# Optimization experiments

Measured on AMD Instinct MI355X. Metric: run time of the kernel, lower is better.

The kernel has to match this reference:

```python
import jax, jax.numpy as jnp
import numpy as np

D_MODEL = 1024
N_HEADS = 16


def setup_inputs() -> dict:
    key = jax.random.key(0)
    ks = jax.random.split(key, 11)
    B, L, D = 2, 2048, D_MODEL
    s = 1.0 / np.sqrt(D)
    return {
        "q": jax.random.normal(ks[0], (B, L, D), jnp.float32),
        "k": jax.random.normal(ks[1], (B, L, D), jnp.float32),
        "v": jax.random.normal(ks[2], (B, L, D), jnp.float32),
        "w_q": jax.random.normal(ks[3], (D, D), jnp.float32) * s,
        "b_q": jnp.zeros((D,), jnp.float32),
        "w_k": jax.random.normal(ks[4], (D, D), jnp.float32) * s,
        "b_k": jnp.zeros((D,), jnp.float32),
        "w_v": jax.random.normal(ks[5], (D, D), jnp.float32) * s,
        "b_v": jnp.zeros((D,), jnp.float32),
        "w_o": jax.random.normal(ks[6], (D, D), jnp.float32) * s,
        "b_o": jnp.zeros((D,), jnp.float32),
    }


def reference(q, k, v, w_q, b_q, w_k, b_k, w_v, b_v, w_o, b_o):
    B, L, D = q.shape
    H = N_HEADS
    d_h = D // H
    # QKV projections (nn.Linear: x @ W^T + b)
    qh = (q @ w_q.T + b_q).reshape(B, L, H, d_h).transpose(0, 2, 1, 3)  # [B,H,L,d_h]
    kh = (k @ w_k.T + b_k).reshape(B, L, H, d_h).transpose(0, 2, 1, 3)
    vh = (v @ w_v.T + b_v).reshape(B, L, H, d_h).transpose(0, 2, 1, 3)
    # scaled dot-product attention
    scores = jnp.einsum('bhqd,bhkd->bhqk', qh, kh) / jnp.sqrt(jnp.float32(d_h))
    attn = jax.nn.softmax(scores, axis=-1)                               # [B,H,L,L]
    ctx = jnp.einsum('bhqk,bhkd->bhqd', attn, vh)                        # [B,H,L,d_h]
    ctx = ctx.transpose(0, 2, 1, 3).reshape(B, L, D)
    out = ctx @ w_o.T + b_o
    return out, attn
```

## Files before the change

### kernel.cpp

```cpp
#include <hip/hip_runtime.h>
#include <hip/hip_bf16.h>
#include <stdint.h>

#define DEV static __device__ __forceinline__

typedef float f32x4 __attribute__((ext_vector_type(4)));
typedef __bf16 bf16x8 __attribute__((ext_vector_type(8)));
typedef unsigned short u16x8 __attribute__((ext_vector_type(8)));
typedef unsigned short u16x4 __attribute__((ext_vector_type(4)));
typedef uint32_t u32x2 __attribute__((ext_vector_type(2)));
typedef unsigned short u16;

#define B_ 2
#define L_ 2048
#define D_MODEL_ 1024
#define H_ 16
#define DH_ 64

#define SHIFT2 11.5415603f

DEV u16 f2bf(float f) {
  union { float f; uint32_t u; } v; v.f = f;
  uint32_t r = v.u + 0x7FFFu + ((v.u >> 16) & 1u);
  return (u16)(r >> 16);
}

DEV float exp2v(float x) {
#if __has_builtin(__builtin_amdgcn_exp2f)
  return __builtin_amdgcn_exp2f(x);
#else
  float r;
  asm("v_exp_f32 %0, %1" : "=v"(r) : "v"(x));
  return r;
#endif
}

DEV uint32_t pkbf(float a, float b) {
  __hip_bfloat162 h = __float22bfloat162_rn(float2{a, b});
  union { __hip_bfloat162 h; uint32_t u; } cv; cv.h = h;
  return cv.u;
}

DEV f32x4 mfma16(bf16x8 a, bf16x8 b, f32x4 c) {
  return __builtin_amdgcn_mfma_f32_16x16x32_bf16(a, b, c, 0, 0, 0);
}

DEV void gl_lds16(const void* g, void* l) {
  __builtin_amdgcn_global_load_lds(
      (const __attribute__((address_space(1))) unsigned int*)g,
      (__attribute__((address_space(3))) unsigned int*)l, 16, 0, 0);
}

struct CastArgs {
  const float* src[7];
  u16* dst[7];
  int n8[7];
};

__global__ __launch_bounds__(256) void cast_kernel(CastArgs a) {
  const int z = blockIdx.z;
  const float* s = a.src[z];
  u16* d = a.dst[z];
  const int n8 = a.n8[z];
  const int stride = gridDim.x * blockDim.x;
  for (int i = blockIdx.x * blockDim.x + threadIdx.x; i < n8; i += stride) {
    const float4* sp = (const float4*)s + (size_t)i * 2;
    float4 x0 = sp[0], x1 = sp[1];
    u16x8 o;
    o[0] = f2bf(x0.x); o[1] = f2bf(x0.y); o[2] = f2bf(x0.z); o[3] = f2bf(x0.w);
    o[4] = f2bf(x1.x); o[5] = f2bf(x1.y); o[6] = f2bf(x1.z); o[7] = f2bf(x1.w);
    *((u16x8*)d + i) = o;
  }
}

#define GM 4096
#define GN 1024
#define GK 1024

struct GemmArgs {
  const u16* X[3];
  const u16* W[3];
  const float* bias[3];
  void* out[3];
  float alpha[3];
  int mode[3];
};

__global__ __launch_bounds__(256) void gemm_bt(GemmArgs g) {
  const int z = blockIdx.z;
  const u16* X = g.X[z];
  const u16* W = g.W[z];
  const float* bias = g.bias[z];
  const float alpha = g.alpha[z];
  const int mode = g.mode[z];
  const int m0 = blockIdx.y * 128, n0 = blockIdx.x * 128;

  __shared__ __align__(16) char smem[32 * 1024];
  char* As = smem;
  char* Bs = smem + 16 * 1024;

  const int tid = threadIdx.x;
  const int lane = tid & 63, w = tid >> 6;
  const int l15 = lane & 15, l4 = lane >> 4;
  const int wm = (w >> 1) * 64, wn = (w & 1) * 64;

  f32x4 acc[4][4];
#pragma unroll
  for (int i = 0; i < 4; ++i)
#pragma unroll
    for (int j = 0; j < 4; ++j) acc[i][j] = f32x4{0.f, 0.f, 0.f, 0.f};

  for (int ks = 0; ks < GK; ks += 64) {
    __syncthreads();
    for (int c = w; c < 16; c += 4) {
      int r = c * 8 + (lane >> 3);
      int j = lane & 7;
      int sj = j ^ (r & 7);
      gl_lds16((const char*)(X + (size_t)(m0 + r) * GK + ks) + sj * 16, As + c * 1024);
      gl_lds16((const char*)(W + (size_t)(n0 + r) * GK + ks) + sj * 16, Bs + c * 1024);
    }
    __syncthreads();
#pragma unroll
    for (int ksub = 0; ksub < 2; ++ksub) {
      bf16x8 af[4], bfr[4];
#pragma unroll
      for (int mf = 0; mf < 4; ++mf) {
        int r = wm + mf * 16 + l15;
        int j16 = ksub * 4 + l4;
        af[mf] = *(const bf16x8*)(As + r * 128 + ((j16 ^ (r & 7)) * 16));
      }
#pragma unroll
      for (int nf = 0; nf < 4; ++nf) {
        int r = wn + nf * 16 + l15;
        int j16 = ksub * 4 + l4;
        bfr[nf] = *(const bf16x8*)(Bs + r * 128 + ((j16 ^ (r & 7)) * 16));
      }
#pragma unroll
      for (int mf = 0; mf < 4; ++mf)
#pragma unroll
        for (int nf = 0; nf < 4; ++nf) acc[mf][nf] = mfma16(af[mf], bfr[nf], acc[mf][nf]);
    }
  }

  if (mode == 2) {
    u16* base = (u16*)g.out[z];
#pragma unroll
    for (int nf = 0; nf < 4; ++nf) {
      int n = n0 + wn + nf * 16 + l15;
      float bv = bias[n];
#pragma unroll
      for (int mf = 0; mf < 4; ++mf) {
        int m = m0 + wm + mf * 16 + l4 * 4;
        u16x4 pk;
#pragma unroll
        for (int r = 0; r < 4; ++r) pk[r] = f2bf((acc[mf][nf][r] + bv) * alpha);
        size_t off = (((size_t)(m >> 11) * H_ + (n >> 6)) * DH_ + (n & 63)) * (size_t)L_ + (m & 2047);
        *(u16x4*)(base + off) = pk;
      }
    }
  } else {
#pragma unroll
    for (int nf = 0; nf < 4; ++nf) {
      int n = n0 + wn + nf * 16 + l15;
      float bv = bias[n];
#pragma unroll
      for (int mf = 0; mf < 4; ++mf) {
#pragma unroll
        for (int r = 0; r < 4; ++r) {
          int m = m0 + wm + mf * 16 + l4 * 4 + r;
          float val = (acc[mf][nf][r] + bv) * alpha;
          if (mode == 1)
            ((float*)g.out[z])[(size_t)m * GN + n] = val;
          else
            ((u16*)g.out[z])[(size_t)m * GN + n] = f2bf(val);
        }
      }
    }
  }
}

__global__ __launch_bounds__(256) void attn_kernel(const u16* Qp, const u16* Kp,
                                                   const u16* VT, float* attn,
                                                   u16* ctx) {
  const int q0 = blockIdx.x * 64;
  const int h = blockIdx.y, b = blockIdx.z;
  const int tid = threadIdx.x, lane = tid & 63, w = tid >> 6;
  const int l15 = lane & 15, l4 = lane >> 4;
  const int lr = lane >> 3, lj = lane & 7;

  __shared__ __align__(16) char smem[48 * 1024];
  char* Qs = smem;
  char* Ps = smem + 8192;

  const u16* Qbase = Qp + ((size_t)(b * L_ + q0) * D_MODEL_ + h * DH_);
  const u16* Kbase = Kp + ((size_t)(b * L_) * D_MODEL_ + h * DH_);
  const u16* VTb = VT + ((size_t)((b * H_ + h) * DH_) * L_);
  float* attnb = attn + ((size_t)(b * H_ + h)) * L_ * L_;

  auto stK = [&](int t) {
    const int c0 = t * 64, bsel = (t & 1) << 13;
    for (int c = w; c < 8; c += 4) {
      int r = c * 8 + lr, sj = lj ^ (r & 7);
      gl_lds16((const char*)(Kbase + (size_t)(c0 + r) * D_MODEL_) + sj * 16,
               smem + 16384 + bsel + c * 1024);
    }
  };
  auto stV = [&](int t) {
    const int c0 = t * 64, bsel = (t & 1) << 13;
    for (int c = w; c < 8; c += 4) {
      int r = c * 8 + lr, sj = lj ^ (r & 7);
      gl_lds16((const char*)(VTb + (size_t)r * L_ + c0) + sj * 16,
               smem + 32768 + bsel + c * 1024);
    }
  };

  for (int c = w; c < 8; c += 4) {
    int r = c * 8 + lr, sj = lj ^ (r & 7);
    gl_lds16((const char*)(Qbase + (size_t)r * D_MODEL_) + sj * 16, Qs + c * 1024);
  }
  stK(0);
  __syncthreads();

  bf16x8 qa[2];
#pragma unroll
  for (int ksub = 0; ksub < 2; ++ksub) {
    int r = w * 16 + l15;
    int j16 = ksub * 4 + l4;
    qa[ksub] = *(const bf16x8*)(Qs + r * 128 + ((j16 ^ (r & 7)) * 16));
  }

  float ssum = 0.f;
  for (int t = 0; t < 32; ++t) {
    if (t < 31) stK(t + 1);
    const char* Ks = smem + 16384 + ((t & 1) << 13);
    f32x4 s[4];
#pragma unroll
    for (int nf = 0; nf < 4; ++nf) s[nf] = f32x4{0.f, 0.f, 0.f, 0.f};
    __builtin_amdgcn_s_setprio(1);
#pragma unroll
    for (int ksub = 0; ksub < 2; ++ksub) {
      int j16 = ksub * 4 + l4;
      bf16x8 kb[4];
#pragma unroll
      for (int nf = 0; nf < 4; ++nf) {
        int r = nf * 16 + l15;
        kb[nf] = *(const bf16x8*)(Ks + r * 128 + ((j16 ^ (r & 7)) * 16));
      }
#pragma unroll
      for (int nf = 0; nf < 4; ++nf) s[nf] = mfma16(kb[nf], qa[ksub], s[nf]);
    }
    __builtin_amdgcn_s_setprio(0);
#pragma unroll
    for (int nf = 0; nf < 4; ++nf)
#pragma unroll
      for (int r = 0; r < 4; ++r) ssum += exp2v(s[nf][r] - SHIFT2);
    __syncthreads();
  }

  stK(0);
  stV(0);

  ssum += __shfl_xor(ssum, 16);
  ssum += __shfl_xor(ssum, 32);
  const float c2 = SHIFT2 + __log2f(ssum);

  f32x4 cacc[4];
#pragma unroll
  for (int i = 0; i < 4; ++i) cacc[i] = f32x4{0.f, 0.f, 0.f, 0.f};
  __syncthreads();

  const int rowq = w * 16 + l15;
  char* PsRow = Ps + rowq * 128;
  float* arow = attnb + (size_t)(q0 + rowq) * L_ + 4 * l4;

  for (int t = 0; t < 32; ++t) {
    if (t < 31) { stK(t + 1); stV(t + 1); }
    const char* Ks = smem + 16384 + ((t & 1) << 13);
    const char* Vs = smem + 32768 + ((t & 1) << 13);
    const int c0 = t * 64;
    f32x4 s[4];
#pragma unroll
    for (int nf = 0; nf < 4; ++nf) s[nf] = f32x4{0.f, 0.f, 0.f, 0.f};
    __builtin_amdgcn_s_setprio(1);
#pragma unroll
    for (int ksub = 0; ksub < 2; ++ksub) {
      int j16 = ksub * 4 + l4;
      bf16x8 kb[4];
#pragma unroll
      for (int nf = 0; nf < 4; ++nf) {
        int r = nf * 16 + l15;
        kb[nf] = *(const bf16x8*)(Ks + r * 128 + ((j16 ^ (r & 7)) * 16));
      }
#pragma unroll
      for (int nf = 0; nf < 4; ++nf) s[nf] = mfma16(kb[nf], qa[ksub], s[nf]);
    }
    __builtin_amdgcn_s_setprio(0);
#pragma unroll
    for (int nf = 0; nf < 4; ++nf) {
      float p0 = exp2v(s[nf][0] - c2);
      float p1 = exp2v(s[nf][1] - c2);
      float p2 = exp2v(s[nf][2] - c2);
      float p3 = exp2v(s[nf][3] - c2);
      f32x4 p4 = {p0, p1, p2, p3};
      __builtin_nontemporal_store(p4, (f32x4*)(arow + c0 + 16 * nf));
      int off = nf * 32 + l4 * 8;
      int chunk = (off >> 4) ^ (rowq & 7);
      u32x2 pk;
      pk[0] = pkbf(p0, p1);
      pk[1] = pkbf(p2, p3);
      *(u32x2*)(PsRow + chunk * 16 + (off & 15)) = pk;
    }
    __builtin_amdgcn_s_setprio(1);
#pragma unroll
    for (int ksub = 0; ksub < 2; ++ksub) {
      int j16 = ksub * 4 + l4;
      bf16x8 pa = *(const bf16x8*)(PsRow + ((j16 ^ (rowq & 7)) * 16));
#pragma unroll
      for (int df = 0; df < 4; ++df) {
        int r = df * 16 + l15;
        bf16x8 vb = *(const bf16x8*)(Vs + r * 128 + ((j16 ^ (r & 7)) * 16));
        cacc[df] = mfma16(pa, vb, cacc[df]);
      }
    }
    __builtin_amdgcn_s_setprio(0);
    __syncthreads();
  }

#pragma unroll
  for (int df = 0; df < 4; ++df) {
#pragma unroll
    for (int r = 0; r < 4; ++r) {
      int row = q0 + w * 16 + l4 * 4 + r;
      int col = h * DH_ + df * 16 + l15;
      ctx[(size_t)(b * L_ + row) * D_MODEL_ + col] = f2bf(cacc[df][r]);
    }
  }
}

extern "C" void kernel_launch(void* const* d_in, const int* in_sizes, int n_in,
                              void* d_out, int out_size, void* d_ws, size_t ws_size,
                              hipStream_t stream) {
  const float* q = (const float*)d_in[0];
  const float* k = (const float*)d_in[1];
  const float* v = (const float*)d_in[2];
  const float* w_q = (const float*)d_in[3];
  const float* b_q = (const float*)d_in[4];
  const float* w_k = (const float*)d_in[5];
  const float* b_k = (const float*)d_in[6];
  const float* w_v = (const float*)d_in[7];
  const float* b_v = (const float*)d_in[8];
  const float* w_o = (const float*)d_in[9];
  const float* b_o = (const float*)d_in[10];

  float* out = (float*)d_out;
  float* attn = (float*)d_out + (size_t)B_ * L_ * D_MODEL_;

  const size_t MB = 1u << 20;
  char* ws = (char*)d_ws;
  u16* qb = (u16*)(ws + 0 * MB);
  u16* kb = (u16*)(ws + 8 * MB);
  u16* vb = (u16*)(ws + 16 * MB);
  u16* wqb = (u16*)(ws + 24 * MB);
  u16* wkb = (u16*)(ws + 26 * MB);
  u16* wvb = (u16*)(ws + 28 * MB);
  u16* wob = (u16*)(ws + 30 * MB);
  u16* Qp = (u16*)(ws + 32 * MB);
  u16* Kp = (u16*)(ws + 40 * MB);
  u16* VT = (u16*)(ws + 48 * MB);
  u16* ctx = kb;

  CastArgs ca;
  ca.src[0] = q;   ca.dst[0] = qb;  ca.n8[0] = (B_ * L_ * D_MODEL_) / 8;
  ca.src[1] = k;   ca.dst[1] = kb;  ca.n8[1] = (B_ * L_ * D_MODEL_) / 8;
  ca.src[2] = v;   ca.dst[2] = vb;  ca.n8[2] = (B_ * L_ * D_MODEL_) / 8;
  ca.src[3] = w_q; ca.dst[3] = wqb; ca.n8[3] = (D_MODEL_ * D_MODEL_) / 8;
  ca.src[4] = w_k; ca.dst[4] = wkb; ca.n8[4] = (D_MODEL_ * D_MODEL_) / 8;
  ca.src[5] = w_v; ca.dst[5] = wvb; ca.n8[5] = (D_MODEL_ * D_MODEL_) / 8;
  ca.src[6] = w_o; ca.dst[6] = wob; ca.n8[6] = (D_MODEL_ * D_MODEL_) / 8;
  cast_kernel<<<dim3(1024, 1, 7), 256, 0, stream>>>(ca);

  GemmArgs ga;
  ga.X[0] = qb;  ga.W[0] = wqb; ga.bias[0] = b_q; ga.out[0] = Qp; ga.alpha[0] = 0.125f * 1.44269504f; ga.mode[0] = 0;
  ga.X[1] = kb;  ga.W[1] = wkb; ga.bias[1] = b_k; ga.out[1] = Kp; ga.alpha[1] = 1.f;    ga.mode[1] = 0;
  ga.X[2] = vb;  ga.W[2] = wvb; ga.bias[2] = b_v; ga.out[2] = VT; ga.alpha[2] = 1.f;    ga.mode[2] = 2;
  gemm_bt<<<dim3(8, 32, 3), 256, 0, stream>>>(ga);

  attn_kernel<<<dim3(32, 16, 2), 256, 0, stream>>>(Qp, Kp, VT, attn, ctx);

  GemmArgs go;
  go.X[0] = ctx; go.W[0] = wob; go.bias[0] = b_o; go.out[0] = out; go.alpha[0] = 1.f; go.mode[0] = 1;
  go.X[1] = ctx; go.W[1] = wob; go.bias[1] = b_o; go.out[1] = out; go.alpha[1] = 1.f; go.mode[1] = 1;
  go.X[2] = ctx; go.W[2] = wob; go.bias[2] = b_o; go.out[2] = out; go.alpha[2] = 1.f; go.mode[2] = 1;
  gemm_bt<<<dim3(8, 32, 1), 256, 0, stream>>>(go);
}
```

Measured before the change: 286.5 us.

## Load K/V tiles directly from global into registers and remap blocks by XCD

The attention kernel stops staging Q, K and V tiles through shared memory with async global-to-LDS copies and double buffering. Each wave now loads its MFMA operands straight from global memory (L2) into registers, which removes all block-level barriers and cuts LDS use to 8 KB, used only for the per-wave P tile. The grid is flattened and remapped so that consecutive blocks on the same XCD share a head and batch, aiming for better L2 reuse of K/V. The costs are redundant global loads across the four waves and uncoalesced 16-byte row reads, with less latency hiding, though occupancy may rise.

After: 444.4 us. 1.55x slower.

```diff
diff --git a/kernel.cpp b/kernel.cpp
--- a/kernel.cpp
+++ b/kernel.cpp
@@ -182,83 +182,53 @@
 __global__ __launch_bounds__(256) void attn_kernel(const u16* Qp, const u16* Kp,
                                                    const u16* VT, float* attn,
                                                    u16* ctx) {
-  const int q0 = blockIdx.x * 64;
-  const int h = blockIdx.y, b = blockIdx.z;
+  const int hid = blockIdx.x;
+  const int lid = (hid & 7) * 128 + (hid >> 3);
+  const int q0 = (lid & 31) * 64;
+  const int h = (lid >> 5) & 15;
+  const int b = lid >> 9;
+
   const int tid = threadIdx.x, lane = tid & 63, w = tid >> 6;
   const int l15 = lane & 15, l4 = lane >> 4;
-  const int lr = lane >> 3, lj = lane & 7;
-
-  __shared__ __align__(16) char smem[48 * 1024];
-  char* Qs = smem;
-  char* Ps = smem + 8192;
-
-  const u16* Qbase = Qp + ((size_t)(b * L_ + q0) * D_MODEL_ + h * DH_);
-  const u16* Kbase = Kp + ((size_t)(b * L_) * D_MODEL_ + h * DH_);
-  const u16* VTb = VT + ((size_t)((b * H_ + h) * DH_) * L_);
+
+  __shared__ __align__(16) char smem[8192];
+  char* PsRow = smem + w * 2048 + l15 * 128;
+  const int swz = l15 & 7;
+
+  const u16* Qbase = Qp + ((size_t)(b * L_ + q0 + w * 16) * D_MODEL_ + h * DH_);
+  const u16* Kb = Kp + ((size_t)(b * L_) * D_MODEL_ + h * DH_);
+  const u16* Vb = VT + ((size_t)((b * H_ + h) * DH_) * L_);
   float* attnb = attn + ((size_t)(b * H_ + h)) * L_ * L_;
 
-  auto stK = [&](int t) {
-    const int c0 = t * 64, bsel = (t & 1) << 13;
-    for (int c = w; c < 8; c += 4) {
-      int r = c * 8 + lr, sj = lj ^ (r & 7);
-      gl_lds16((const char*)(Kbase + (size_t)(c0 + r) * D_MODEL_) + sj * 16,
-               smem + 16384 + bsel + c * 1024);
-    }
-  };
-  auto stV = [&](int t) {
-    const int c0 = t * 64, bsel = (t & 1) << 13;
-    for (int c = w; c < 8; c += 4) {
-      int r = c * 8 + lr, sj = lj ^ (r & 7);
-      gl_lds16((const char*)(VTb + (size_t)r * L_ + c0) + sj * 16,
-               smem + 32768 + bsel + c * 1024);
-    }
-  };
-
-  for (int c = w; c < 8; c += 4) {
-    int r = c * 8 + lr, sj = lj ^ (r & 7);
-    gl_lds16((const char*)(Qbase + (size_t)r * D_MODEL_) + sj * 16, Qs + c * 1024);
-  }
-  stK(0);
-  __syncthreads();
-
   bf16x8 qa[2];
 #pragma unroll
-  for (int ksub = 0; ksub < 2; ++ksub) {
-    int r = w * 16 + l15;
-    int j16 = ksub * 4 + l4;
-    qa[ksub] = *(const bf16x8*)(Qs + r * 128 + ((j16 ^ (r & 7)) * 16));
-  }
+  for (int ksub = 0; ksub < 2; ++ksub)
+    qa[ksub] = *(const bf16x8*)(Qbase + (size_t)l15 * D_MODEL_ + (ksub * 4 + l4) * 8);
 
   float ssum = 0.f;
   for (int t = 0; t < 32; ++t) {
-    if (t < 31) stK(t + 1);
-    const char* Ks = smem + 16384 + ((t & 1) << 13);
+    const u16* Kt = Kb + (size_t)t * 64 * D_MODEL_;
+    bf16x8 kb[2][4];
+#pragma unroll
+    for (int ksub = 0; ksub < 2; ++ksub)
+#pragma unroll
+      for (int nf = 0; nf < 4; ++nf)
+        kb[ksub][nf] = *(const bf16x8*)(Kt + (size_t)(nf * 16 + l15) * D_MODEL_ +
+                                        (ksub * 4 + l4) * 8);
     f32x4 s[4];
 #pragma unroll
     for (int nf = 0; nf < 4; ++nf) s[nf] = f32x4{0.f, 0.f, 0.f, 0.f};
     __builtin_amdgcn_s_setprio(1);
 #pragma unroll
-    for (int ksub = 0; ksub < 2; ++ksub) {
-      int j16 = ksub * 4 + l4;
-      bf16x8 kb[4];
-#pragma unroll
-      for (int nf = 0; nf < 4; ++nf) {
-        int r = nf * 16 + l15;
-        kb[nf] = *(const bf16x8*)(Ks + r * 128 + ((j16 ^ (r & 7)) * 16));
-      }
-#pragma unroll
-      for (int nf = 0; nf < 4; ++nf) s[nf] = mfma16(kb[nf], qa[ksub], s[nf]);
-    }
+    for (int ksub = 0; ksub < 2; ++ksub)
+#pragma unroll
+      for (int nf = 0; nf < 4; ++nf) s[nf] = mfma16(kb[ksub][nf], qa[ksub], s[nf]);
     __builtin_amdgcn_s_setprio(0);
 #pragma unroll
     for (int nf = 0; nf < 4; ++nf)
 #pragma unroll
       for (int r = 0; r < 4; ++r) ssum += exp2v(s[nf][r] - SHIFT2);
-    __syncthreads();
-  }
-
-  stK(0);
-  stV(0);
+  }
 
   ssum += __shfl_xor(ssum, 16);
   ssum += __shfl_xor(ssum, 32);
@@ -267,33 +237,30 @@
   f32x4 cacc[4];
 #pragma unroll
   for (int i = 0; i < 4; ++i) cacc[i] = f32x4{0.f, 0.f, 0.f, 0.f};
-  __syncthreads();
-
-  const int rowq = w * 16 + l15;
-  char* PsRow = Ps + rowq * 128;
-  float* arow = attnb + (size_t)(q0 + rowq) * L_ + 4 * l4;
+
+  float* arow = attnb + (size_t)(q0 + w * 16 + l15) * L_ + 4 * l4;
 
   for (int t = 0; t < 32; ++t) {
-    if (t < 31) { stK(t + 1); stV(t + 1); }
-    const char* Ks = smem + 16384 + ((t & 1) << 13);
-    const char* Vs = smem + 32768 + ((t & 1) << 13);
     const int c0 = t * 64;
+    const u16* Kt = Kb + (size_t)c0 * D_MODEL_;
+    bf16x8 kb[2][4], vbr[2][4];
+#pragma unroll
+    for (int ksub = 0; ksub < 2; ++ksub)
+#pragma unroll
+      for (int nf = 0; nf < 4; ++nf) {
+        kb[ksub][nf] = *(const bf16x8*)(Kt + (size_t)(nf * 16 + l15) * D_MODEL_ +
+                                        (ksub * 4 + l4) * 8);
+        vbr[ksub][nf] = *(const bf16x8*)(Vb + (size_t)(nf * 16 + l15) * L_ + c0 +
+                                         (ksub * 4 + l4) * 8);
+      }
     f32x4 s[4];
 #pragma unroll
     for (int nf = 0; nf < 4; ++nf) s[nf] = f32x4{0.f, 0.f, 0.f, 0.f};
     __builtin_amdgcn_s_setprio(1);
 #pragma unroll
-    for (int ksub = 0; ksub < 2; ++ksub) {
-      int j16 = ksub * 4 + l4;
-      bf16x8 kb[4];
-#pragma unroll
-      for (int nf = 0; nf < 4; ++nf) {
-        int r = nf * 16 + l15;
-        kb[nf] = *(const bf16x8*)(Ks + r * 128 + ((j16 ^ (r & 7)) * 16));
-      }
-#pragma unroll
-      for (int nf = 0; nf < 4; ++nf) s[nf] = mfma16(kb[nf], qa[ksub], s[nf]);
-    }
+    for (int ksub = 0; ksub < 2; ++ksub)
+#pragma unroll
+      for (int nf = 0; nf < 4; ++nf) s[nf] = mfma16(kb[ksub][nf], qa[ksub], s[nf]);
     __builtin_amdgcn_s_setprio(0);
 #pragma unroll
     for (int nf = 0; nf < 4; ++nf) {
@@ -304,7 +271,7 @@
       f32x4 p4 = {p0, p1, p2, p3};
       __builtin_nontemporal_store(p4, (f32x4*)(arow + c0 + 16 * nf));
       int off = nf * 32 + l4 * 8;
-      int chunk = (off >> 4) ^ (rowq & 7);
+      int chunk = (off >> 4) ^ swz;
       u32x2 pk;
       pk[0] = pkbf(p0, p1);
       pk[1] = pkbf(p2, p3);
@@ -314,16 +281,12 @@
 #pragma unroll
     for (int ksub = 0; ksub < 2; ++ksub) {
       int j16 = ksub * 4 + l4;
-      bf16x8 pa = *(const bf16x8*)(PsRow + ((j16 ^ (rowq & 7)) * 16));
-#pragma unroll
-      for (int df = 0; df < 4; ++df) {
-        int r = df * 16 + l15;
-        bf16x8 vb = *(const bf16x8*)(Vs + r * 128 + ((j16 ^ (r & 7)) * 16));
-        cacc[df] = mfma16(pa, vb, cacc[df]);
-      }
+      bf16x8 pa = *(const bf16x8*)(smem + w * 2048 + l15 * 128 + ((j16 ^ swz) * 16));
+#pragma unroll
+      for (int df = 0; df < 4; ++df)
+        cacc[df] = mfma16(pa, vbr[ksub][df], cacc[df]);
     }
     __builtin_amdgcn_s_setprio(0);
-    __syncthreads();
   }
 
 #pragma unroll
@@ -385,7 +348,7 @@
   ga.X[2] = vb;  ga.W[2] = wvb; ga.bias[2] = b_v; ga.out[2] = VT; ga.alpha[2] = 1.f;    ga.mode[2] = 2;
   gemm_bt<<<dim3(8, 32, 3), 256, 0, stream>>>(ga);
 
-  attn_kernel<<<dim3(32, 16, 2), 256, 0, stream>>>(Qp, Kp, VT, attn, ctx);
+  attn_kernel<<<dim3(1024, 1, 1), 256, 0, stream>>>(Qp, Kp, VT, attn, ctx);
 
   GemmArgs go;
   go.X[0] = ctx; go.W[0] = wob; go.bias[0] = b_o; go.out[0] = out; go.alpha[0] = 1.f; go.mode[0] = 1;
```
